# Optimization experiments

Hardware: AMD Instinct MI355X
Metric: run time of the kernel (lower is better)

## Reference

```python
import jax, jax.numpy as jnp
import numpy as np

T, D, H, O = 1048576, 64, 128, 32  # tokens, input_size, expert hidden, expert output_size


def setup_inputs() -> dict:
    key = jax.random.key(0)
    ks = jax.random.split(key, 11)
    s = 0.02
    return {
        "x": jax.random.normal(ks[0], (T, D), dtype=jnp.float32),
        "topk_idx": jax.random.randint(ks[1], (T, 2), 0, 2),
        "weights": jax.random.uniform(ks[2], (T, 2), dtype=jnp.float32),
        # expert 0: MLP D -> H -> O
        "W0a": jax.random.normal(ks[3], (D, H), dtype=jnp.float32) * s,
        "b0a": jnp.zeros((H,), dtype=jnp.float32),
        "W0b": jax.random.normal(ks[4], (H, O), dtype=jnp.float32) * s,
        "b0b": jnp.zeros((O,), dtype=jnp.float32),
        # expert 1: MLP (D + O) -> H -> O  (memory-enhanced input)
        "W1a": jax.random.normal(ks[5], (D + O, H), dtype=jnp.float32) * s,
        "b1a": jnp.zeros((H,), dtype=jnp.float32),
        "W1b": jax.random.normal(ks[6], (H, O), dtype=jnp.float32) * s,
        "b1b": jnp.zeros((O,), dtype=jnp.float32),
    }


def reference(x, topk_idx, weights, W0a, b0a, W0b, b0b, W1a, b1a, W1b, b1b):
    mask0 = (topk_idx == 0).any(axis=1)  # [T]
    mask1 = (topk_idx == 1).any(axis=1)  # [T]

    # expert 0 output, zero where not routed (matches zeros buffer + masked scatter)
    e0 = jnp.maximum(x @ W0a + b0a, 0.0) @ W0b + b0b      # [T, O]
    out0 = jnp.where(mask0[:, None], e0, 0.0)

    # last_valid_fill: forward-fill last valid row index (invalid -> 0, then cummax)
    t = jnp.arange(T)
    idx = jax.lax.cummax(jnp.where(mask0, t, 0))           # [T] int
    filled = out0[idx]                                     # [T, O] gather rows

    # expert 1 on [x, last_valid_out0], zero where not routed
    x1 = jnp.concatenate([x, filled], axis=1)              # [T, D+O]
    e1 = jnp.maximum(x1 @ W1a + b1a, 0.0) @ W1b + b1b      # [T, O]
    out1 = jnp.where(mask1[:, None], e1, 0.0)

    w = weights[:, :1]                                     # [T, 1]
    return w * out0 + (1.0 - w) * out1
```

## Files before the change

kernel.cpp:

```cpp
#include <hip/hip_runtime.h>
#include <hip/hip_bf16.h>

#define TROWS 1048576
#define RPB   256
#define NCHUNK (TROWS / RPB)
#define LSTRIDE 36

typedef float f32x4  __attribute__((ext_vector_type(4)));
typedef short bf16x8 __attribute__((ext_vector_type(8)));
typedef short bf16x4 __attribute__((ext_vector_type(4)));

#define MFMA(a, b, c) __builtin_amdgcn_mfma_f32_16x16x32_bf16(a, b, c, 0, 0, 0)

__device__ __forceinline__ short f2bf(float v) {
    __hip_bfloat16 b = __float2bfloat16(v);
    return __builtin_bit_cast(short, b);
}
__device__ __forceinline__ float bf2f(short s) {
    unsigned u = ((unsigned)(unsigned short)s) << 16;
    return __builtin_bit_cast(float, u);
}

__global__ __launch_bounds__(64) void prep_kernel(
    const float* __restrict__ W0a, const float* __restrict__ W0b,
    const float* __restrict__ W1a, const float* __restrict__ W1b,
    bf16x8* __restrict__ frag)
{
    const int fid = blockIdx.x, l = threadIdx.x, c = l & 15, g = l >> 4;
    const float* W; int N, ks, nt;
    if (fid < 16)      { W = W0a; N = 128; ks = fid >> 3;        nt = fid & 7; }
    else if (fid < 24) { W = W0b; N = 32;  ks = (fid - 16) >> 1; nt = (fid - 16) & 1; }
    else if (fid < 48) { W = W1a; N = 128; ks = (fid - 24) >> 3; nt = (fid - 24) & 7; }
    else               { W = W1b; N = 32;  ks = (fid - 48) >> 1; nt = (fid - 48) & 1; }
    bf16x8 f;
    #pragma unroll
    for (int j = 0; j < 8; ++j) {
        const int k = 32 * ks + ((j < 4) ? (4 * g + j) : (16 + 4 * g + (j - 4)));
        f[j] = f2bf(W[k * N + 16 * nt + c]);
    }
    frag[fid * 64 + l] = f;
}

__global__ __launch_bounds__(256, 3) void fused_kernel(
    const float* __restrict__ x, const int* __restrict__ topk,
    const float* __restrict__ wts,
    const float* __restrict__ b0a, const float* __restrict__ b0b,
    const float* __restrict__ b1a, const float* __restrict__ b1b,
    const bf16x8* __restrict__ frag,
    float* __restrict__ out)
{
    const int b = blockIdx.x;
    const int bb = b * RPB;
    const int tid = threadIdx.x, wv = tid >> 6, l = tid & 63, c = l & 15, g = l >> 4;

    __shared__ __align__(16) short frag_lds[32 * 64 * 8];
    __shared__ __align__(16) short out0_lds[257 * LSTRIDE];
    __shared__ int wtot[4];

    #define LDSF(fl) (*(const bf16x8*)&frag_lds[(((fl) * 64) + l) * 8])

    #pragma unroll
    for (int i = 0; i < 6; ++i) {
        const int e = tid + i * 256;
        *(f32x4*)&frag_lds[e * 8] = *(const f32x4*)&frag[e];
    }

    const int t = bb + tid;
    const int2 tko = ((const int2*)topk)[t];
    const bool m0o = (tko.x == 0) || (tko.y == 0);
    const bool m1o = (tko.x == 1) || (tko.y == 1);
    const int  mo_own   = (m0o ? 1 : 0) | (m1o ? 2 : 0);
    const float wgt_own = wts[(size_t)t * 2];

    int s = m0o ? t : 0;
    #pragma unroll
    for (int off = 1; off < 64; off <<= 1) {
        int u = __shfl_up(s, off, 64);
        if (l >= off) s = max(s, u);
    }
    if (l == 63) wtot[wv] = s;

    int p = 0;
    for (int base = bb - 64; base >= 0; base -= 64) {
        const int2 tkq = ((const int2*)topk)[base + l];
        const bool mm = (tkq.x == 0) || (tkq.y == 0);
        const unsigned long long bal = __ballot(mm);
        if (bal) { p = base + 63 - __clzll(bal); break; }
    }
    const int2 tkp = ((const int2*)topk)[p];
    const bool m0p = (tkp.x == 0) || (tkp.y == 0);

    bf16x8 xf[4][2];
    #pragma unroll
    for (int rt = 0; rt < 4; ++rt) {
        const int row = bb + wv * 64 + rt * 16 + c;
        const float* xr = x + (size_t)row * 64;
        #pragma unroll
        for (int ks = 0; ks < 2; ++ks) {
            f32x4 a  = *(const f32x4*)(xr + 32 * ks + 4 * g);
            f32x4 b2 = *(const f32x4*)(xr + 32 * ks + 16 + 4 * g);
            #pragma unroll
            for (int j = 0; j < 4; ++j) { xf[rt][ks][j] = f2bf(a[j]); xf[rt][ks][4 + j] = f2bf(b2[j]); }
        }
    }
    bf16x8 xfp[2];
    if (wv == 3) {
        const float* xp = x + (size_t)p * 64;
        #pragma unroll
        for (int ks = 0; ks < 2; ++ks) {
            f32x4 a  = *(const f32x4*)(xp + 32 * ks + 4 * g);
            f32x4 b2 = *(const f32x4*)(xp + 32 * ks + 16 + 4 * g);
            #pragma unroll
            for (int j = 0; j < 4; ++j) { xfp[ks][j] = f2bf(a[j]); xfp[ks][4 + j] = f2bf(b2[j]); }
        }
    }

    __syncthreads();

    int pre = 0;
    #pragma unroll
    for (int w2 = 0; w2 < 4; ++w2)
        if (w2 < wv) pre = max(pre, wtot[w2]);
    const int s_full = max(pre, s);

    f32x4 acc2a[4][2];
    {
        f32x4 bi0 = *(const f32x4*)(b0b + 4 * g);
        f32x4 bi1 = *(const f32x4*)(b0b + 16 + 4 * g);
        #pragma unroll
        for (int rt = 0; rt < 4; ++rt) { acc2a[rt][0] = bi0; acc2a[rt][1] = bi1; }
    }
    __builtin_amdgcn_s_setprio(1);
    #pragma unroll
    for (int k2 = 0; k2 < 4; ++k2) {
        const bf16x8 fa00 = LDSF(0 * 8 + 2 * k2 + 0);
        const bf16x8 fa01 = LDSF(0 * 8 + 2 * k2 + 1);
        const bf16x8 fa10 = LDSF(1 * 8 + 2 * k2 + 0);
        const bf16x8 fa11 = LDSF(1 * 8 + 2 * k2 + 1);
        const bf16x8 fb0  = LDSF(16 + 2 * k2 + 0);
        const bf16x8 fb1  = LDSF(16 + 2 * k2 + 1);
        const f32x4 bi0 = *(const f32x4*)(b0a + 16 * (2 * k2 + 0) + 4 * g);
        const f32x4 bi1 = *(const f32x4*)(b0a + 16 * (2 * k2 + 1) + 4 * g);
        #pragma unroll
        for (int rt = 0; rt < 4; ++rt) {
            f32x4 a10 = bi0, a11 = bi1;
            a10 = MFMA(fa00, xf[rt][0], a10);
            a10 = MFMA(fa10, xf[rt][1], a10);
            a11 = MFMA(fa01, xf[rt][0], a11);
            a11 = MFMA(fa11, xf[rt][1], a11);
            bf16x8 hf;
            #pragma unroll
            for (int j = 0; j < 8; ++j)
                hf[j] = f2bf(fmaxf((j < 4 ? a10 : a11)[j & 3], 0.0f));
            acc2a[rt][0] = MFMA(fb0, hf, acc2a[rt][0]);
            acc2a[rt][1] = MFMA(fb1, hf, acc2a[rt][1]);
        }
    }
    __builtin_amdgcn_s_setprio(0);

    #pragma unroll
    for (int rt = 0; rt < 4; ++rt) {
        const int slot = wv * 64 + rt * 16 + c;
        const bool m0 = (__shfl(mo_own, rt * 16 + c, 64) & 1);
        #pragma unroll
        for (int ot = 0; ot < 2; ++ot) {
            bf16x4 v;
            #pragma unroll
            for (int j = 0; j < 4; ++j) v[j] = f2bf(m0 ? acc2a[rt][ot][j] : 0.0f);
            *(bf16x4*)(&out0_lds[slot * LSTRIDE + 16 * ot + 4 * g]) = v;
        }
    }

    if (wv == 3) {
        f32x4 accp[2];
        accp[0] = *(const f32x4*)(b0b + 4 * g);
        accp[1] = *(const f32x4*)(b0b + 16 + 4 * g);
        #pragma unroll
        for (int k2 = 0; k2 < 4; ++k2) {
            const bf16x8 fa00 = LDSF(0 * 8 + 2 * k2 + 0);
            const bf16x8 fa01 = LDSF(0 * 8 + 2 * k2 + 1);
            const bf16x8 fa10 = LDSF(1 * 8 + 2 * k2 + 0);
            const bf16x8 fa11 = LDSF(1 * 8 + 2 * k2 + 1);
            const bf16x8 fb0  = LDSF(16 + 2 * k2 + 0);
            const bf16x8 fb1  = LDSF(16 + 2 * k2 + 1);
            f32x4 a10 = *(const f32x4*)(b0a + 16 * (2 * k2 + 0) + 4 * g);
            f32x4 a11 = *(const f32x4*)(b0a + 16 * (2 * k2 + 1) + 4 * g);
            a10 = MFMA(fa00, xfp[0], a10);
            a10 = MFMA(fa10, xfp[1], a10);
            a11 = MFMA(fa01, xfp[0], a11);
            a11 = MFMA(fa11, xfp[1], a11);
            bf16x8 hf;
            #pragma unroll
            for (int j = 0; j < 8; ++j)
                hf[j] = f2bf(fmaxf((j < 4 ? a10 : a11)[j & 3], 0.0f));
            accp[0] = MFMA(fb0, hf, accp[0]);
            accp[1] = MFMA(fb1, hf, accp[1]);
        }
        if (c == 0) {
            #pragma unroll
            for (int ot = 0; ot < 2; ++ot) {
                bf16x4 v;
                #pragma unroll
                for (int j = 0; j < 4; ++j) v[j] = f2bf(m0p ? accp[ot][j] : 0.0f);
                *(bf16x4*)(&out0_lds[256 * LSTRIDE + 16 * ot + 4 * g]) = v;
            }
        }
    }

    __syncthreads();

    bf16x8 xf2[4];
    #pragma unroll
    for (int rt = 0; rt < 4; ++rt) {
        const int sF = __shfl(s_full, rt * 16 + c, 64);
        const int slot = (sF > 0) ? (sF - bb) : 256;
        const short* fr = &out0_lds[slot * LSTRIDE];
        bf16x4 fa_ = *(const bf16x4*)(fr + 4 * g);
        bf16x4 fb_ = *(const bf16x4*)(fr + 16 + 4 * g);
        #pragma unroll
        for (int j = 0; j < 4; ++j) { xf2[rt][j] = fa_[j]; xf2[rt][4 + j] = fb_[j]; }
    }

    #pragma unroll
    for (int i = 0; i < 8; ++i) {
        const int e = tid + i * 256;
        *(f32x4*)&frag_lds[e * 8] = *(const f32x4*)&frag[24 * 64 + e];
    }

    __syncthreads();

    f32x4 acc2b[4][2];
    {
        f32x4 bi0 = *(const f32x4*)(b1b + 4 * g);
        f32x4 bi1 = *(const f32x4*)(b1b + 16 + 4 * g);
        #pragma unroll
        for (int rt = 0; rt < 4; ++rt) { acc2b[rt][0] = bi0; acc2b[rt][1] = bi1; }
    }
    __builtin_amdgcn_s_setprio(1);
    #pragma unroll
    for (int k2 = 0; k2 < 4; ++k2) {
        const bf16x8 fa00 = LDSF(0 * 8 + 2 * k2 + 0);
        const bf16x8 fa01 = LDSF(0 * 8 + 2 * k2 + 1);
        const bf16x8 fa10 = LDSF(1 * 8 + 2 * k2 + 0);
        const bf16x8 fa11 = LDSF(1 * 8 + 2 * k2 + 1);
        const bf16x8 fa20 = LDSF(2 * 8 + 2 * k2 + 0);
        const bf16x8 fa21 = LDSF(2 * 8 + 2 * k2 + 1);
        const bf16x8 fb0  = LDSF(24 + 2 * k2 + 0);
        const bf16x8 fb1  = LDSF(24 + 2 * k2 + 1);
        const f32x4 bi0 = *(const f32x4*)(b1a + 16 * (2 * k2 + 0) + 4 * g);
        const f32x4 bi1 = *(const f32x4*)(b1a + 16 * (2 * k2 + 1) + 4 * g);
        #pragma unroll
        for (int rt = 0; rt < 4; ++rt) {
            f32x4 a10 = bi0, a11 = bi1;
            a10 = MFMA(fa00, xf[rt][0], a10);
            a10 = MFMA(fa10, xf[rt][1], a10);
            a10 = MFMA(fa20, xf2[rt], a10);
            a11 = MFMA(fa01, xf[rt][0], a11);
            a11 = MFMA(fa11, xf[rt][1], a11);
            a11 = MFMA(fa21, xf2[rt], a11);
            bf16x8 hf;
            #pragma unroll
            for (int j = 0; j < 8; ++j)
                hf[j] = f2bf(fmaxf((j < 4 ? a10 : a11)[j & 3], 0.0f));
            acc2b[rt][0] = MFMA(fb0, hf, acc2b[rt][0]);
            acc2b[rt][1] = MFMA(fb1, hf, acc2b[rt][1]);
        }
    }
    __builtin_amdgcn_s_setprio(0);

    #pragma unroll
    for (int rt = 0; rt < 4; ++rt) {
        const int slot = wv * 64 + rt * 16 + c;
        const int row = bb + slot;
        const int mo   = __shfl(mo_own, rt * 16 + c, 64);
        const float w  = __shfl(wgt_own, rt * 16 + c, 64);
        const float wc = 1.0f - w;
        const bool m1 = mo & 2;
        #pragma unroll
        for (int ot = 0; ot < 2; ++ot) {
            bf16x4 oa = *(const bf16x4*)(&out0_lds[slot * LSTRIDE + 16 * ot + 4 * g]);
            f32x4 r;
            #pragma unroll
            for (int j = 0; j < 4; ++j) {
                const float e1 = m1 ? acc2b[rt][ot][j] : 0.0f;
                r[j] = w * bf2f(oa[j]) + wc * e1;
            }
            *(f32x4*)(out + (size_t)row * 32 + 16 * ot + 4 * g) = r;
        }
    }
    #undef LDSF
}

extern "C" void kernel_launch(void* const* d_in, const int* in_sizes, int n_in,
                              void* d_out, int out_size, void* d_ws, size_t ws_size,
                              hipStream_t stream)
{
    const float* x    = (const float*)d_in[0];
    const int*   topk = (const int*)  d_in[1];
    const float* wts  = (const float*)d_in[2];
    const float* W0a  = (const float*)d_in[3];
    const float* b0a  = (const float*)d_in[4];
    const float* W0b  = (const float*)d_in[5];
    const float* b0b  = (const float*)d_in[6];
    const float* W1a  = (const float*)d_in[7];
    const float* b1a  = (const float*)d_in[8];
    const float* W1b  = (const float*)d_in[9];
    const float* b1b  = (const float*)d_in[10];
    float* out = (float*)d_out;

    bf16x8* frag = (bf16x8*)d_ws;

    prep_kernel<<<dim3(56), dim3(64), 0, stream>>>(W0a, W0b, W1a, W1b, frag);
    fused_kernel<<<dim3(NCHUNK), dim3(256), 0, stream>>>(
        x, topk, wts, b0a, b0b, b1a, b1b, frag, out);
}
```

Before: 137.2 us.

## Halve rows per block, swizzle out0 LDS, fold carry-row MLP into main loop

Each block now handles 128 rows instead of 256, so each wave owns 32 rows. Occupancy is raised to 4 blocks per CU and LDS use shrinks: the out0 buffer becomes a 32-wide XOR-swizzled layout with no padding, and slot 0 is reused for the carried-in row. The expert-0 computation for the previous block's last valid row is interleaved into the main k-loop instead of running afterwards. Expert-1 weights are prefetched into registers before the barrier, and the feature rows are read from LDS inside the loop. Other changes: the k-loops are no longer unrolled, setprio is dropped, and the per-wave scan totals share storage with out0_lds. That aliasing risks a race between reading the totals and other waves writing out0.

```diff
diff --git a/kernel.cpp b/kernel.cpp
--- a/kernel.cpp
+++ b/kernel.cpp
@@ -2,9 +2,8 @@
 #include <hip/hip_bf16.h>
 
 #define TROWS 1048576
-#define RPB   256
-#define NCHUNK (TROWS / RPB)
-#define LSTRIDE 36
+#define RPB   128
+#define NBLK  (TROWS / RPB)
 
 typedef float f32x4  __attribute__((ext_vector_type(4)));
 typedef short bf16x8 __attribute__((ext_vector_type(8)));
@@ -19,6 +18,9 @@
 __device__ __forceinline__ float bf2f(short s) {
     unsigned u = ((unsigned)(unsigned short)s) << 16;
     return __builtin_bit_cast(float, u);
+}
+__device__ __forceinline__ int o0idx(int slot, int u) {
+    return slot * 32 + ((u ^ (slot & 7)) << 2);
 }
 
 __global__ __launch_bounds__(64) void prep_kernel(
@@ -41,7 +43,7 @@
     frag[fid * 64 + l] = f;
 }
 
-__global__ __launch_bounds__(256, 3) void fused_kernel(
+__global__ __launch_bounds__(256, 4) void fused_kernel(
     const float* __restrict__ x, const int* __restrict__ topk,
     const float* __restrict__ wts,
     const float* __restrict__ b0a, const float* __restrict__ b0b,
@@ -52,10 +54,11 @@
     const int b = blockIdx.x;
     const int bb = b * RPB;
     const int tid = threadIdx.x, wv = tid >> 6, l = tid & 63, c = l & 15, g = l >> 4;
-
-    __shared__ __align__(16) short frag_lds[32 * 64 * 8];
-    __shared__ __align__(16) short out0_lds[257 * LSTRIDE];
-    __shared__ int wtot[4];
+    const int rr = l & 31;
+
+    __shared__ __align__(16) short frag_lds[2048 * 16 / 2];
+    __shared__ __align__(16) short out0_lds[128 * 32];
+    int* wtot = (int*)out0_lds;
 
     #define LDSF(fl) (*(const bf16x8*)&frag_lds[(((fl) * 64) + l) * 8])
 
@@ -65,20 +68,23 @@
         *(f32x4*)&frag_lds[e * 8] = *(const f32x4*)&frag[e];
     }
 
-    const int t = bb + tid;
-    const int2 tko = ((const int2*)topk)[t];
+    const int srow = bb + wv * 32 + rr;
+    const int2 tko = ((const int2*)topk)[srow];
     const bool m0o = (tko.x == 0) || (tko.y == 0);
     const bool m1o = (tko.x == 1) || (tko.y == 1);
     const int  mo_own   = (m0o ? 1 : 0) | (m1o ? 2 : 0);
-    const float wgt_own = wts[(size_t)t * 2];
-
-    int s = m0o ? t : 0;
-    #pragma unroll
-    for (int off = 1; off < 64; off <<= 1) {
-        int u = __shfl_up(s, off, 64);
-        if (l >= off) s = max(s, u);
-    }
-    if (l == 63) wtot[wv] = s;
+    const float wgt_own = wts[(size_t)srow * 2];
+
+    int s = m0o ? srow : 0;
+    #pragma unroll
+    for (int off = 1; off < 32; off <<= 1) {
+        int u = __shfl_up(s, off, 32);
+        if (rr >= off) s = max(s, u);
+    }
+    if (l == 31) wtot[wv] = s;
+
+    const int2 tk0 = ((const int2*)topk)[bb];
+    const bool m0row0 = (tk0.x == 0) || (tk0.y == 0);
 
     int p = 0;
     for (int base = bb - 64; base >= 0; base -= 64) {
@@ -90,10 +96,10 @@
     const int2 tkp = ((const int2*)topk)[p];
     const bool m0p = (tkp.x == 0) || (tkp.y == 0);
 
-    bf16x8 xf[4][2];
-    #pragma unroll
-    for (int rt = 0; rt < 4; ++rt) {
-        const int row = bb + wv * 64 + rt * 16 + c;
+    bf16x8 xf[2][2];
+    #pragma unroll
+    for (int rt = 0; rt < 2; ++rt) {
+        const int row = bb + wv * 32 + rt * 16 + c;
         const float* xr = x + (size_t)row * 64;
         #pragma unroll
         for (int ks = 0; ks < 2; ++ks) {
@@ -123,15 +129,15 @@
         if (w2 < wv) pre = max(pre, wtot[w2]);
     const int s_full = max(pre, s);
 
-    f32x4 acc2a[4][2];
+    f32x4 acc2a[2][2], accp[2];
     {
         f32x4 bi0 = *(const f32x4*)(b0b + 4 * g);
         f32x4 bi1 = *(const f32x4*)(b0b + 16 + 4 * g);
-        #pragma unroll
-        for (int rt = 0; rt < 4; ++rt) { acc2a[rt][0] = bi0; acc2a[rt][1] = bi1; }
-    }
-    __builtin_amdgcn_s_setprio(1);
-    #pragma unroll
+        acc2a[0][0] = bi0; acc2a[0][1] = bi1;
+        acc2a[1][0] = bi0; acc2a[1][1] = bi1;
+        accp[0] = bi0; accp[1] = bi1;
+    }
+    #pragma unroll 1
     for (int k2 = 0; k2 < 4; ++k2) {
         const bf16x8 fa00 = LDSF(0 * 8 + 2 * k2 + 0);
         const bf16x8 fa01 = LDSF(0 * 8 + 2 * k2 + 1);
@@ -142,7 +148,7 @@
         const f32x4 bi0 = *(const f32x4*)(b0a + 16 * (2 * k2 + 0) + 4 * g);
         const f32x4 bi1 = *(const f32x4*)(b0a + 16 * (2 * k2 + 1) + 4 * g);
         #pragma unroll
-        for (int rt = 0; rt < 4; ++rt) {
+        for (int rt = 0; rt < 2; ++rt) {
             f32x4 a10 = bi0, a11 = bi1;
             a10 = MFMA(fa00, xf[rt][0], a10);
             a10 = MFMA(fa10, xf[rt][1], a10);
@@ -155,36 +161,8 @@
             acc2a[rt][0] = MFMA(fb0, hf, acc2a[rt][0]);
             acc2a[rt][1] = MFMA(fb1, hf, acc2a[rt][1]);
         }
-    }
-    __builtin_amdgcn_s_setprio(0);
-
-    #pragma unroll
-    for (int rt = 0; rt < 4; ++rt) {
-        const int slot = wv * 64 + rt * 16 + c;
-        const bool m0 = (__shfl(mo_own, rt * 16 + c, 64) & 1);
-        #pragma unroll
-        for (int ot = 0; ot < 2; ++ot) {
-            bf16x4 v;
-            #pragma unroll
-            for (int j = 0; j < 4; ++j) v[j] = f2bf(m0 ? acc2a[rt][ot][j] : 0.0f);
-            *(bf16x4*)(&out0_lds[slot * LSTRIDE + 16 * ot + 4 * g]) = v;
-        }
-    }
-
-    if (wv == 3) {
-        f32x4 accp[2];
-        accp[0] = *(const f32x4*)(b0b + 4 * g);
-        accp[1] = *(const f32x4*)(b0b + 16 + 4 * g);
-        #pragma unroll
-        for (int k2 = 0; k2 < 4; ++k2) {
-            const bf16x8 fa00 = LDSF(0 * 8 + 2 * k2 + 0);
-            const bf16x8 fa01 = LDSF(0 * 8 + 2 * k2 + 1);
-            const bf16x8 fa10 = LDSF(1 * 8 + 2 * k2 + 0);
-            const bf16x8 fa11 = LDSF(1 * 8 + 2 * k2 + 1);
-            const bf16x8 fb0  = LDSF(16 + 2 * k2 + 0);
-            const bf16x8 fb1  = LDSF(16 + 2 * k2 + 1);
-            f32x4 a10 = *(const f32x4*)(b0a + 16 * (2 * k2 + 0) + 4 * g);
-            f32x4 a11 = *(const f32x4*)(b0a + 16 * (2 * k2 + 1) + 4 * g);
+        if (wv == 3) {
+            f32x4 a10 = bi0, a11 = bi1;
             a10 = MFMA(fa00, xfp[0], a10);
             a10 = MFMA(fa10, xfp[1], a10);
             a11 = MFMA(fa01, xfp[0], a11);
@@ -196,48 +174,68 @@
             accp[0] = MFMA(fb0, hf, accp[0]);
             accp[1] = MFMA(fb1, hf, accp[1]);
         }
-        if (c == 0) {
-            #pragma unroll
-            for (int ot = 0; ot < 2; ++ot) {
-                bf16x4 v;
-                #pragma unroll
-                for (int j = 0; j < 4; ++j) v[j] = f2bf(m0p ? accp[ot][j] : 0.0f);
-                *(bf16x4*)(&out0_lds[256 * LSTRIDE + 16 * ot + 4 * g]) = v;
-            }
+    }
+
+    #pragma unroll
+    for (int rt = 0; rt < 2; ++rt) {
+        const int slot = wv * 32 + rt * 16 + c;
+        const bool m0 = (__shfl(mo_own, rt * 16 + c, 64) & 1);
+        const bool sk = (slot == 0) && !m0row0;
+        #pragma unroll
+        for (int ot = 0; ot < 2; ++ot) {
+            bf16x4 v;
+            #pragma unroll
+            for (int j = 0; j < 4; ++j) v[j] = f2bf(m0 ? acc2a[rt][ot][j] : 0.0f);
+            if (!sk) *(bf16x4*)(&out0_lds[o0idx(slot, ot * 4 + g)]) = v;
+        }
+    }
+    if (wv == 3 && !m0row0 && c == 0) {
+        #pragma unroll
+        for (int ot = 0; ot < 2; ++ot) {
+            bf16x4 v;
+            #pragma unroll
+            for (int j = 0; j < 4; ++j) v[j] = f2bf(m0p ? accp[ot][j] : 0.0f);
+            *(bf16x4*)(&out0_lds[o0idx(0, ot * 4 + g)]) = v;
         }
     }
 
     __syncthreads();
 
-    bf16x8 xf2[4];
-    #pragma unroll
-    for (int rt = 0; rt < 4; ++rt) {
+    f32x4 w1t0 = *(const f32x4*)&frag[24 * 64 + tid + 0 * 256];
+    f32x4 w1t1 = *(const f32x4*)&frag[24 * 64 + tid + 1 * 256];
+    f32x4 w1t2 = *(const f32x4*)&frag[24 * 64 + tid + 2 * 256];
+    f32x4 w1t3 = *(const f32x4*)&frag[24 * 64 + tid + 3 * 256];
+    f32x4 w1t4 = *(const f32x4*)&frag[24 * 64 + tid + 4 * 256];
+    f32x4 w1t5 = *(const f32x4*)&frag[24 * 64 + tid + 5 * 256];
+    f32x4 w1t6 = *(const f32x4*)&frag[24 * 64 + tid + 6 * 256];
+    f32x4 w1t7 = *(const f32x4*)&frag[24 * 64 + tid + 7 * 256];
+
+    int slotF[2];
+    #pragma unroll
+    for (int rt = 0; rt < 2; ++rt) {
         const int sF = __shfl(s_full, rt * 16 + c, 64);
-        const int slot = (sF > 0) ? (sF - bb) : 256;
-        const short* fr = &out0_lds[slot * LSTRIDE];
-        bf16x4 fa_ = *(const bf16x4*)(fr + 4 * g);
-        bf16x4 fb_ = *(const bf16x4*)(fr + 16 + 4 * g);
-        #pragma unroll
-        for (int j = 0; j < 4; ++j) { xf2[rt][j] = fa_[j]; xf2[rt][4 + j] = fb_[j]; }
-    }
-
-    #pragma unroll
-    for (int i = 0; i < 8; ++i) {
-        const int e = tid + i * 256;
-        *(f32x4*)&frag_lds[e * 8] = *(const f32x4*)&frag[24 * 64 + e];
-    }
+        slotF[rt] = (sF > 0) ? (sF - bb) : 0;
+    }
+
+    *(f32x4*)&frag_lds[(tid + 0 * 256) * 8] = w1t0;
+    *(f32x4*)&frag_lds[(tid + 1 * 256) * 8] = w1t1;
+    *(f32x4*)&frag_lds[(tid + 2 * 256) * 8] = w1t2;
+    *(f32x4*)&frag_lds[(tid + 3 * 256) * 8] = w1t3;
+    *(f32x4*)&frag_lds[(tid + 4 * 256) * 8] = w1t4;
+    *(f32x4*)&frag_lds[(tid + 5 * 256) * 8] = w1t5;
+    *(f32x4*)&frag_lds[(tid + 6 * 256) * 8] = w1t6;
+    *(f32x4*)&frag_lds[(tid + 7 * 256) * 8] = w1t7;
 
     __syncthreads();
 
-    f32x4 acc2b[4][2];
+    f32x4 acc2b[2][2];
     {
         f32x4 bi0 = *(const f32x4*)(b1b + 4 * g);
         f32x4 bi1 = *(const f32x4*)(b1b + 16 + 4 * g);
-        #pragma unroll
-        for (int rt = 0; rt < 4; ++rt) { acc2b[rt][0] = bi0; acc2b[rt][1] = bi1; }
-    }
-    __builtin_amdgcn_s_setprio(1);
-    #pragma unroll
+        acc2b[0][0] = bi0; acc2b[0][1] = bi1;
+        acc2b[1][0] = bi0; acc2b[1][1] = bi1;
+    }
+    #pragma unroll 1
     for (int k2 = 0; k2 < 4; ++k2) {
         const bf16x8 fa00 = LDSF(0 * 8 + 2 * k2 + 0);
         const bf16x8 fa01 = LDSF(0 * 8 + 2 * k2 + 1);
@@ -250,14 +248,22 @@
         const f32x4 bi0 = *(const f32x4*)(b1a + 16 * (2 * k2 + 0) + 4 * g);
         const f32x4 bi1 = *(const f32x4*)(b1a + 16 * (2 * k2 + 1) + 4 * g);
         #pragma unroll
-        for (int rt = 0; rt < 4; ++rt) {
+        for (int rt = 0; rt < 2; ++rt) {
+            bf16x8 xf2;
+            {
+                const int sl = slotF[rt];
+                bf16x4 fa_ = *(const bf16x4*)&out0_lds[o0idx(sl, g)];
+                bf16x4 fb_ = *(const bf16x4*)&out0_lds[o0idx(sl, 4 + g)];
+                #pragma unroll
+                for (int j = 0; j < 4; ++j) { xf2[j] = fa_[j]; xf2[4 + j] = fb_[j]; }
+            }
             f32x4 a10 = bi0, a11 = bi1;
             a10 = MFMA(fa00, xf[rt][0], a10);
             a10 = MFMA(fa10, xf[rt][1], a10);
-            a10 = MFMA(fa20, xf2[rt], a10);
+            a10 = MFMA(fa20, xf2, a10);
             a11 = MFMA(fa01, xf[rt][0], a11);
             a11 = MFMA(fa11, xf[rt][1], a11);
-            a11 = MFMA(fa21, xf2[rt], a11);
+            a11 = MFMA(fa21, xf2, a11);
             bf16x8 hf;
             #pragma unroll
             for (int j = 0; j < 8; ++j)
@@ -266,24 +272,25 @@
             acc2b[rt][1] = MFMA(fb1, hf, acc2b[rt][1]);
         }
     }
-    __builtin_amdgcn_s_setprio(0);
-
-    #pragma unroll
-    for (int rt = 0; rt < 4; ++rt) {
-        const int slot = wv * 64 + rt * 16 + c;
+
+    #pragma unroll
+    for (int rt = 0; rt < 2; ++rt) {
+        const int slot = wv * 32 + rt * 16 + c;
         const int row = bb + slot;
         const int mo   = __shfl(mo_own, rt * 16 + c, 64);
         const float w  = __shfl(wgt_own, rt * 16 + c, 64);
         const float wc = 1.0f - w;
         const bool m1 = mo & 2;
+        const bool kill = (slot == 0) && !m0row0;
         #pragma unroll
         for (int ot = 0; ot < 2; ++ot) {
-            bf16x4 oa = *(const bf16x4*)(&out0_lds[slot * LSTRIDE + 16 * ot + 4 * g]);
+            bf16x4 oa = *(const bf16x4*)(&out0_lds[o0idx(slot, ot * 4 + g)]);
             f32x4 r;
             #pragma unroll
             for (int j = 0; j < 4; ++j) {
+                const float e0 = kill ? 0.0f : bf2f(oa[j]);
                 const float e1 = m1 ? acc2b[rt][ot][j] : 0.0f;
-                r[j] = w * bf2f(oa[j]) + wc * e1;
+                r[j] = w * e0 + wc * e1;
             }
             *(f32x4*)(out + (size_t)row * 32 + 16 * ot + 4 * g) = r;
         }
@@ -311,6 +318,6 @@
     bf16x8* frag = (bf16x8*)d_ws;
 
     prep_kernel<<<dim3(56), dim3(64), 0, stream>>>(W0a, W0b, W1a, W1b, frag);
-    fused_kernel<<<dim3(NCHUNK), dim3(256), 0, stream>>>(
+    fused_kernel<<<dim3(NBLK), dim3(256), 0, stream>>>(
         x, topk, wts, b0a, b0b, b1a, b1b, frag, out);
 }
```

Measured after the change: 134.3 us. 2.1% less time.

## Make fused kernel persistent over 8 chunks with register prefetch and carried fill index

Applied to the files above, without the earlier changes.

Each block now processes 8 consecutive 256-row chunks instead of one. All weight fragments for both experts are loaded into LDS once per block. The next chunk's x, topk and weights are prefetched into registers while the current chunk computes. The backward scan for the last valid expert-0 row is done once per block, and the fill index is then carried from chunk to chunk. This removes the repeated per-chunk scans, weight reloads and a sync, but raises register and LDS pressure (occupancy hint drops to 2) and gives only 512 blocks.

```diff
diff --git a/kernel.cpp b/kernel.cpp
--- a/kernel.cpp
+++ b/kernel.cpp
@@ -2,8 +2,9 @@
 #include <hip/hip_bf16.h>
 
 #define TROWS 1048576
-#define RPB   256
-#define NCHUNK (TROWS / RPB)
+#define RPC   256
+#define CPB   8
+#define NBLK  (TROWS / (RPC * CPB))
 #define LSTRIDE 36
 
 typedef float f32x4  __attribute__((ext_vector_type(4)));
@@ -41,7 +42,7 @@
     frag[fid * 64 + l] = f;
 }
 
-__global__ __launch_bounds__(256, 3) void fused_kernel(
+__global__ __launch_bounds__(256, 2) void fused_kernel(
     const float* __restrict__ x, const int* __restrict__ topk,
     const float* __restrict__ wts,
     const float* __restrict__ b0a, const float* __restrict__ b0b,
@@ -49,132 +50,96 @@
     const bf16x8* __restrict__ frag,
     float* __restrict__ out)
 {
-    const int b = blockIdx.x;
-    const int bb = b * RPB;
     const int tid = threadIdx.x, wv = tid >> 6, l = tid & 63, c = l & 15, g = l >> 4;
-
-    __shared__ __align__(16) short frag_lds[32 * 64 * 8];
+    const int blk0 = blockIdx.x * (RPC * CPB);
+
+    __shared__ __align__(16) short frag_lds[56 * 64 * 8];
     __shared__ __align__(16) short out0_lds[257 * LSTRIDE];
     __shared__ int wtot[4];
 
-    #define LDSF(fl) (*(const bf16x8*)&frag_lds[(((fl) * 64) + l) * 8])
+    #define LDSF(fid_) (*(const bf16x8*)&frag_lds[(((fid_) * 64) + l) * 8])
 
     #pragma unroll
-    for (int i = 0; i < 6; ++i) {
-        const int e = tid + i * 256;
-        *(f32x4*)&frag_lds[e * 8] = *(const f32x4*)&frag[e];
+    for (int i = 0; i < 14; ++i)
+        *(f32x4*)&frag_lds[(tid + i * 256) * 8] = *(const f32x4*)&frag[tid + i * 256];
+
+    int p = 0; bool m0p = false;
+    f32x4 xpraw[4];
+    if (wv == 3) {
+        for (int base = blk0 - 64; base >= 0; base -= 64) {
+            const int2 tkq = ((const int2*)topk)[base + l];
+            const bool mm = (tkq.x == 0) || (tkq.y == 0);
+            const unsigned long long bal = __ballot(mm);
+            if (bal) { p = base + 63 - __clzll(bal); break; }
+        }
+        const int2 tkp = ((const int2*)topk)[p];
+        m0p = (tkp.x == 0) || (tkp.y == 0);
+        const float* xp = x + (size_t)p * 64;
+        xpraw[0] = *(const f32x4*)(xp + 4 * g);
+        xpraw[1] = *(const f32x4*)(xp + 16 + 4 * g);
+        xpraw[2] = *(const f32x4*)(xp + 32 + 4 * g);
+        xpraw[3] = *(const f32x4*)(xp + 48 + 4 * g);
     }
 
-    const int t = bb + tid;
-    const int2 tko = ((const int2*)topk)[t];
-    const bool m0o = (tko.x == 0) || (tko.y == 0);
-    const bool m1o = (tko.x == 1) || (tko.y == 1);
-    const int  mo_own   = (m0o ? 1 : 0) | (m1o ? 2 : 0);
-    const float wgt_own = wts[(size_t)t * 2];
-
-    int s = m0o ? t : 0;
-    #pragma unroll
-    for (int off = 1; off < 64; off <<= 1) {
-        int u = __shfl_up(s, off, 64);
-        if (l >= off) s = max(s, u);
-    }
-    if (l == 63) wtot[wv] = s;
-
-    int p = 0;
-    for (int base = bb - 64; base >= 0; base -= 64) {
-        const int2 tkq = ((const int2*)topk)[base + l];
-        const bool mm = (tkq.x == 0) || (tkq.y == 0);
-        const unsigned long long bal = __ballot(mm);
-        if (bal) { p = base + 63 - __clzll(bal); break; }
-    }
-    const int2 tkp = ((const int2*)topk)[p];
-    const bool m0p = (tkp.x == 0) || (tkp.y == 0);
-
-    bf16x8 xf[4][2];
+    f32x4 xraw[16];
     #pragma unroll
     for (int rt = 0; rt < 4; ++rt) {
-        const int row = bb + wv * 64 + rt * 16 + c;
-        const float* xr = x + (size_t)row * 64;
-        #pragma unroll
-        for (int ks = 0; ks < 2; ++ks) {
-            f32x4 a  = *(const f32x4*)(xr + 32 * ks + 4 * g);
-            f32x4 b2 = *(const f32x4*)(xr + 32 * ks + 16 + 4 * g);
-            #pragma unroll
-            for (int j = 0; j < 4; ++j) { xf[rt][ks][j] = f2bf(a[j]); xf[rt][ks][4 + j] = f2bf(b2[j]); }
-        }
+        const float* xr = x + (size_t)(blk0 + wv * 64 + rt * 16 + c) * 64;
+        xraw[rt * 4 + 0] = *(const f32x4*)(xr + 4 * g);
+        xraw[rt * 4 + 1] = *(const f32x4*)(xr + 16 + 4 * g);
+        xraw[rt * 4 + 2] = *(const f32x4*)(xr + 32 + 4 * g);
+        xraw[rt * 4 + 3] = *(const f32x4*)(xr + 48 + 4 * g);
     }
-    bf16x8 xfp[2];
-    if (wv == 3) {
-        const float* xp = x + (size_t)p * 64;
-        #pragma unroll
-        for (int ks = 0; ks < 2; ++ks) {
-            f32x4 a  = *(const f32x4*)(xp + 32 * ks + 4 * g);
-            f32x4 b2 = *(const f32x4*)(xp + 32 * ks + 16 + 4 * g);
-            #pragma unroll
-            for (int j = 0; j < 4; ++j) { xfp[ks][j] = f2bf(a[j]); xfp[ks][4 + j] = f2bf(b2[j]); }
-        }
-    }
+    int2  tko = ((const int2*)topk)[blk0 + tid];
+    float wgt = wts[(size_t)(blk0 + tid) * 2];
 
     __syncthreads();
 
-    int pre = 0;
-    #pragma unroll
-    for (int w2 = 0; w2 < 4; ++w2)
-        if (w2 < wv) pre = max(pre, wtot[w2]);
-    const int s_full = max(pre, s);
-
-    f32x4 acc2a[4][2];
-    {
-        f32x4 bi0 = *(const f32x4*)(b0b + 4 * g);
-        f32x4 bi1 = *(const f32x4*)(b0b + 16 + 4 * g);
-        #pragma unroll
-        for (int rt = 0; rt < 4; ++rt) { acc2a[rt][0] = bi0; acc2a[rt][1] = bi1; }
-    }
-    __builtin_amdgcn_s_setprio(1);
-    #pragma unroll
-    for (int k2 = 0; k2 < 4; ++k2) {
-        const bf16x8 fa00 = LDSF(0 * 8 + 2 * k2 + 0);
-        const bf16x8 fa01 = LDSF(0 * 8 + 2 * k2 + 1);
-        const bf16x8 fa10 = LDSF(1 * 8 + 2 * k2 + 0);
-        const bf16x8 fa11 = LDSF(1 * 8 + 2 * k2 + 1);
-        const bf16x8 fb0  = LDSF(16 + 2 * k2 + 0);
-        const bf16x8 fb1  = LDSF(16 + 2 * k2 + 1);
-        const f32x4 bi0 = *(const f32x4*)(b0a + 16 * (2 * k2 + 0) + 4 * g);
-        const f32x4 bi1 = *(const f32x4*)(b0a + 16 * (2 * k2 + 1) + 4 * g);
-        #pragma unroll
-        for (int rt = 0; rt < 4; ++rt) {
-            f32x4 a10 = bi0, a11 = bi1;
-            a10 = MFMA(fa00, xf[rt][0], a10);
-            a10 = MFMA(fa10, xf[rt][1], a10);
-            a11 = MFMA(fa01, xf[rt][0], a11);
-            a11 = MFMA(fa11, xf[rt][1], a11);
-            bf16x8 hf;
-            #pragma unroll
-            for (int j = 0; j < 8; ++j)
-                hf[j] = f2bf(fmaxf((j < 4 ? a10 : a11)[j & 3], 0.0f));
-            acc2a[rt][0] = MFMA(fb0, hf, acc2a[rt][0]);
-            acc2a[rt][1] = MFMA(fb1, hf, acc2a[rt][1]);
-        }
-    }
-    __builtin_amdgcn_s_setprio(0);
-
-    #pragma unroll
-    for (int rt = 0; rt < 4; ++rt) {
-        const int slot = wv * 64 + rt * 16 + c;
-        const bool m0 = (__shfl(mo_own, rt * 16 + c, 64) & 1);
-        #pragma unroll
-        for (int ot = 0; ot < 2; ++ot) {
-            bf16x4 v;
-            #pragma unroll
-            for (int j = 0; j < 4; ++j) v[j] = f2bf(m0 ? acc2a[rt][ot][j] : 0.0f);
-            *(bf16x4*)(&out0_lds[slot * LSTRIDE + 16 * ot + 4 * g]) = v;
-        }
-    }
-
-    if (wv == 3) {
-        f32x4 accp[2];
-        accp[0] = *(const f32x4*)(b0b + 4 * g);
-        accp[1] = *(const f32x4*)(b0b + 16 + 4 * g);
+    #pragma unroll 1
+    for (int ch = 0; ch < CPB; ++ch) {
+        const int cb = blk0 + ch * RPC;
+
+        bf16x8 xf[4][2];
+        #pragma unroll
+        for (int rt = 0; rt < 4; ++rt)
+            #pragma unroll
+            for (int ks = 0; ks < 2; ++ks) {
+                const f32x4 a  = xraw[rt * 4 + ks * 2 + 0];
+                const f32x4 b2 = xraw[rt * 4 + ks * 2 + 1];
+                #pragma unroll
+                for (int j = 0; j < 4; ++j) { xf[rt][ks][j] = f2bf(a[j]); xf[rt][ks][4 + j] = f2bf(b2[j]); }
+            }
+        bf16x8 xfp[2];
+        if (wv == 3) {
+            #pragma unroll
+            for (int ks = 0; ks < 2; ++ks) {
+                const f32x4 a  = xpraw[ks * 2 + 0];
+                const f32x4 b2 = xpraw[ks * 2 + 1];
+                #pragma unroll
+                for (int j = 0; j < 4; ++j) { xfp[ks][j] = f2bf(a[j]); xfp[ks][4 + j] = f2bf(b2[j]); }
+            }
+        }
+
+        const bool m0o = (tko.x == 0) || (tko.y == 0);
+        const bool m1o = (tko.x == 1) || (tko.y == 1);
+        const int  mo_own   = (m0o ? 1 : 0) | (m1o ? 2 : 0);
+        const float wgt_own = wgt;
+        int s = m0o ? (cb + tid) : 0;
+        #pragma unroll
+        for (int off = 1; off < 64; off <<= 1) {
+            int u = __shfl_up(s, off, 64);
+            if (l >= off) s = max(s, u);
+        }
+        if (l == 63) wtot[wv] = s;
+
+        f32x4 acc2a[4][2], accp[2];
+        {
+            f32x4 bi0 = *(const f32x4*)(b0b + 4 * g);
+            f32x4 bi1 = *(const f32x4*)(b0b + 16 + 4 * g);
+            #pragma unroll
+            for (int rt = 0; rt < 4; ++rt) { acc2a[rt][0] = bi0; acc2a[rt][1] = bi1; }
+            accp[0] = bi0; accp[1] = bi1;
+        }
         #pragma unroll
         for (int k2 = 0; k2 < 4; ++k2) {
             const bf16x8 fa00 = LDSF(0 * 8 + 2 * k2 + 0);
@@ -183,110 +148,162 @@
             const bf16x8 fa11 = LDSF(1 * 8 + 2 * k2 + 1);
             const bf16x8 fb0  = LDSF(16 + 2 * k2 + 0);
             const bf16x8 fb1  = LDSF(16 + 2 * k2 + 1);
-            f32x4 a10 = *(const f32x4*)(b0a + 16 * (2 * k2 + 0) + 4 * g);
-            f32x4 a11 = *(const f32x4*)(b0a + 16 * (2 * k2 + 1) + 4 * g);
-            a10 = MFMA(fa00, xfp[0], a10);
-            a10 = MFMA(fa10, xfp[1], a10);
-            a11 = MFMA(fa01, xfp[0], a11);
-            a11 = MFMA(fa11, xfp[1], a11);
-            bf16x8 hf;
-            #pragma unroll
-            for (int j = 0; j < 8; ++j)
-                hf[j] = f2bf(fmaxf((j < 4 ? a10 : a11)[j & 3], 0.0f));
-            accp[0] = MFMA(fb0, hf, accp[0]);
-            accp[1] = MFMA(fb1, hf, accp[1]);
-        }
-        if (c == 0) {
+            const f32x4 bi0 = *(const f32x4*)(b0a + 16 * (2 * k2 + 0) + 4 * g);
+            const f32x4 bi1 = *(const f32x4*)(b0a + 16 * (2 * k2 + 1) + 4 * g);
+            #pragma unroll
+            for (int rt = 0; rt < 4; ++rt) {
+                f32x4 a10 = bi0, a11 = bi1;
+                a10 = MFMA(fa00, xf[rt][0], a10);
+                a10 = MFMA(fa10, xf[rt][1], a10);
+                a11 = MFMA(fa01, xf[rt][0], a11);
+                a11 = MFMA(fa11, xf[rt][1], a11);
+                bf16x8 hf;
+                #pragma unroll
+                for (int j = 0; j < 8; ++j)
+                    hf[j] = f2bf(fmaxf((j < 4 ? a10 : a11)[j & 3], 0.0f));
+                acc2a[rt][0] = MFMA(fb0, hf, acc2a[rt][0]);
+                acc2a[rt][1] = MFMA(fb1, hf, acc2a[rt][1]);
+            }
+            if (wv == 3) {
+                f32x4 a10 = bi0, a11 = bi1;
+                a10 = MFMA(fa00, xfp[0], a10);
+                a10 = MFMA(fa10, xfp[1], a10);
+                a11 = MFMA(fa01, xfp[0], a11);
+                a11 = MFMA(fa11, xfp[1], a11);
+                bf16x8 hf;
+                #pragma unroll
+                for (int j = 0; j < 8; ++j)
+                    hf[j] = f2bf(fmaxf((j < 4 ? a10 : a11)[j & 3], 0.0f));
+                accp[0] = MFMA(fb0, hf, accp[0]);
+                accp[1] = MFMA(fb1, hf, accp[1]);
+            }
+        }
+
+        #pragma unroll
+        for (int rt = 0; rt < 4; ++rt) {
+            const int slot = wv * 64 + rt * 16 + c;
+            const bool m0 = (__shfl(mo_own, rt * 16 + c, 64) & 1);
             #pragma unroll
             for (int ot = 0; ot < 2; ++ot) {
                 bf16x4 v;
                 #pragma unroll
+                for (int j = 0; j < 4; ++j) v[j] = f2bf(m0 ? acc2a[rt][ot][j] : 0.0f);
+                *(bf16x4*)(&out0_lds[slot * LSTRIDE + 16 * ot + 4 * g]) = v;
+            }
+        }
+        if (wv == 3 && c == 0) {
+            #pragma unroll
+            for (int ot = 0; ot < 2; ++ot) {
+                bf16x4 v;
+                #pragma unroll
                 for (int j = 0; j < 4; ++j) v[j] = f2bf(m0p ? accp[ot][j] : 0.0f);
                 *(bf16x4*)(&out0_lds[256 * LSTRIDE + 16 * ot + 4 * g]) = v;
             }
         }
-    }
-
-    __syncthreads();
-
-    bf16x8 xf2[4];
-    #pragma unroll
-    for (int rt = 0; rt < 4; ++rt) {
-        const int sF = __shfl(s_full, rt * 16 + c, 64);
-        const int slot = (sF > 0) ? (sF - bb) : 256;
-        const short* fr = &out0_lds[slot * LSTRIDE];
-        bf16x4 fa_ = *(const bf16x4*)(fr + 4 * g);
-        bf16x4 fb_ = *(const bf16x4*)(fr + 16 + 4 * g);
-        #pragma unroll
-        for (int j = 0; j < 4; ++j) { xf2[rt][j] = fa_[j]; xf2[rt][4 + j] = fb_[j]; }
-    }
-
-    #pragma unroll
-    for (int i = 0; i < 8; ++i) {
-        const int e = tid + i * 256;
-        *(f32x4*)&frag_lds[e * 8] = *(const f32x4*)&frag[24 * 64 + e];
-    }
-
-    __syncthreads();
-
-    f32x4 acc2b[4][2];
-    {
-        f32x4 bi0 = *(const f32x4*)(b1b + 4 * g);
-        f32x4 bi1 = *(const f32x4*)(b1b + 16 + 4 * g);
-        #pragma unroll
-        for (int rt = 0; rt < 4; ++rt) { acc2b[rt][0] = bi0; acc2b[rt][1] = bi1; }
-    }
-    __builtin_amdgcn_s_setprio(1);
-    #pragma unroll
-    for (int k2 = 0; k2 < 4; ++k2) {
-        const bf16x8 fa00 = LDSF(0 * 8 + 2 * k2 + 0);
-        const bf16x8 fa01 = LDSF(0 * 8 + 2 * k2 + 1);
-        const bf16x8 fa10 = LDSF(1 * 8 + 2 * k2 + 0);
-        const bf16x8 fa11 = LDSF(1 * 8 + 2 * k2 + 1);
-        const bf16x8 fa20 = LDSF(2 * 8 + 2 * k2 + 0);
-        const bf16x8 fa21 = LDSF(2 * 8 + 2 * k2 + 1);
-        const bf16x8 fb0  = LDSF(24 + 2 * k2 + 0);
-        const bf16x8 fb1  = LDSF(24 + 2 * k2 + 1);
-        const f32x4 bi0 = *(const f32x4*)(b1a + 16 * (2 * k2 + 0) + 4 * g);
-        const f32x4 bi1 = *(const f32x4*)(b1a + 16 * (2 * k2 + 1) + 4 * g);
+
+        __syncthreads();
+
+        if (ch + 1 < CPB) {
+            const int nb = cb + RPC;
+            #pragma unroll
+            for (int rt = 0; rt < 4; ++rt) {
+                const float* xr = x + (size_t)(nb + wv * 64 + rt * 16 + c) * 64;
+                xraw[rt * 4 + 0] = *(const f32x4*)(xr + 4 * g);
+                xraw[rt * 4 + 1] = *(const f32x4*)(xr + 16 + 4 * g);
+                xraw[rt * 4 + 2] = *(const f32x4*)(xr + 32 + 4 * g);
+                xraw[rt * 4 + 3] = *(const f32x4*)(xr + 48 + 4 * g);
+            }
+            tko = ((const int2*)topk)[nb + tid];
+            wgt = wts[(size_t)(nb + tid) * 2];
+        }
+
+        int pre = 0;
+        #pragma unroll
+        for (int w2 = 0; w2 < 4; ++w2)
+            if (w2 < wv) pre = max(pre, wtot[w2]);
+        const int s_full = max(pre, s);
+
+        if (wv == 3 && ch + 1 < CPB) {
+            const int sl = __shfl(s_full, 63, 64);
+            if (sl > 0) { p = sl; m0p = true; }
+            const float* xp = x + (size_t)p * 64;
+            xpraw[0] = *(const f32x4*)(xp + 4 * g);
+            xpraw[1] = *(const f32x4*)(xp + 16 + 4 * g);
+            xpraw[2] = *(const f32x4*)(xp + 32 + 4 * g);
+            xpraw[3] = *(const f32x4*)(xp + 48 + 4 * g);
+        }
+
+        bf16x8 xf2[4];
         #pragma unroll
         for (int rt = 0; rt < 4; ++rt) {
-            f32x4 a10 = bi0, a11 = bi1;
-            a10 = MFMA(fa00, xf[rt][0], a10);
-            a10 = MFMA(fa10, xf[rt][1], a10);
-            a10 = MFMA(fa20, xf2[rt], a10);
-            a11 = MFMA(fa01, xf[rt][0], a11);
-            a11 = MFMA(fa11, xf[rt][1], a11);
-            a11 = MFMA(fa21, xf2[rt], a11);
-            bf16x8 hf;
-            #pragma unroll
-            for (int j = 0; j < 8; ++j)
-                hf[j] = f2bf(fmaxf((j < 4 ? a10 : a11)[j & 3], 0.0f));
-            acc2b[rt][0] = MFMA(fb0, hf, acc2b[rt][0]);
-            acc2b[rt][1] = MFMA(fb1, hf, acc2b[rt][1]);
-        }
-    }
-    __builtin_amdgcn_s_setprio(0);
-
-    #pragma unroll
-    for (int rt = 0; rt < 4; ++rt) {
-        const int slot = wv * 64 + rt * 16 + c;
-        const int row = bb + slot;
-        const int mo   = __shfl(mo_own, rt * 16 + c, 64);
-        const float w  = __shfl(wgt_own, rt * 16 + c, 64);
-        const float wc = 1.0f - w;
-        const bool m1 = mo & 2;
-        #pragma unroll
-        for (int ot = 0; ot < 2; ++ot) {
-            bf16x4 oa = *(const bf16x4*)(&out0_lds[slot * LSTRIDE + 16 * ot + 4 * g]);
-            f32x4 r;
-            #pragma unroll
-            for (int j = 0; j < 4; ++j) {
-                const float e1 = m1 ? acc2b[rt][ot][j] : 0.0f;
-                r[j] = w * bf2f(oa[j]) + wc * e1;
-            }
-            *(f32x4*)(out + (size_t)row * 32 + 16 * ot + 4 * g) = r;
-        }
+            const int sF = __shfl(s_full, rt * 16 + c, 64);
+            const int slot = (sF >= cb) ? (sF - cb) : 256;
+            const short* fr = &out0_lds[slot * LSTRIDE];
+            bf16x4 fa_ = *(const bf16x4*)(fr + 4 * g);
+            bf16x4 fb_ = *(const bf16x4*)(fr + 16 + 4 * g);
+            #pragma unroll
+            for (int j = 0; j < 4; ++j) { xf2[rt][j] = fa_[j]; xf2[rt][4 + j] = fb_[j]; }
+        }
+
+        f32x4 acc2b[4][2];
+        {
+            f32x4 bi0 = *(const f32x4*)(b1b + 4 * g);
+            f32x4 bi1 = *(const f32x4*)(b1b + 16 + 4 * g);
+            #pragma unroll
+            for (int rt = 0; rt < 4; ++rt) { acc2b[rt][0] = bi0; acc2b[rt][1] = bi1; }
+        }
+        #pragma unroll
+        for (int k2 = 0; k2 < 4; ++k2) {
+            const bf16x8 fa00 = LDSF(24 + 0 * 8 + 2 * k2 + 0);
+            const bf16x8 fa01 = LDSF(24 + 0 * 8 + 2 * k2 + 1);
+            const bf16x8 fa10 = LDSF(24 + 1 * 8 + 2 * k2 + 0);
+            const bf16x8 fa11 = LDSF(24 + 1 * 8 + 2 * k2 + 1);
+            const bf16x8 fa20 = LDSF(24 + 2 * 8 + 2 * k2 + 0);
+            const bf16x8 fa21 = LDSF(24 + 2 * 8 + 2 * k2 + 1);
+            const bf16x8 fb0  = LDSF(48 + 2 * k2 + 0);
+            const bf16x8 fb1  = LDSF(48 + 2 * k2 + 1);
+            const f32x4 bi0 = *(const f32x4*)(b1a + 16 * (2 * k2 + 0) + 4 * g);
+            const f32x4 bi1 = *(const f32x4*)(b1a + 16 * (2 * k2 + 1) + 4 * g);
+            #pragma unroll
+            for (int rt = 0; rt < 4; ++rt) {
+                f32x4 a10 = bi0, a11 = bi1;
+                a10 = MFMA(fa00, xf[rt][0], a10);
+                a10 = MFMA(fa10, xf[rt][1], a10);
+                a10 = MFMA(fa20, xf2[rt], a10);
+                a11 = MFMA(fa01, xf[rt][0], a11);
+                a11 = MFMA(fa11, xf[rt][1], a11);
+                a11 = MFMA(fa21, xf2[rt], a11);
+                bf16x8 hf;
+                #pragma unroll
+                for (int j = 0; j < 8; ++j)
+                    hf[j] = f2bf(fmaxf((j < 4 ? a10 : a11)[j & 3], 0.0f));
+                acc2b[rt][0] = MFMA(fb0, hf, acc2b[rt][0]);
+                acc2b[rt][1] = MFMA(fb1, hf, acc2b[rt][1]);
+            }
+        }
+
+        #pragma unroll
+        for (int rt = 0; rt < 4; ++rt) {
+            const int slot = wv * 64 + rt * 16 + c;
+            const int row = cb + slot;
+            const int mo   = __shfl(mo_own, rt * 16 + c, 64);
+            const float w  = __shfl(wgt_own, rt * 16 + c, 64);
+            const float wc = 1.0f - w;
+            const bool m1 = mo & 2;
+            #pragma unroll
+            for (int ot = 0; ot < 2; ++ot) {
+                bf16x4 oa = *(const bf16x4*)(&out0_lds[slot * LSTRIDE + 16 * ot + 4 * g]);
+                f32x4 r;
+                #pragma unroll
+                for (int j = 0; j < 4; ++j) {
+                    const float e1 = m1 ? acc2b[rt][ot][j] : 0.0f;
+                    r[j] = w * bf2f(oa[j]) + wc * e1;
+                }
+                *(f32x4*)(out + (size_t)row * 32 + 16 * ot + 4 * g) = r;
+            }
+        }
+
+        __syncthreads();
     }
     #undef LDSF
 }
@@ -311,6 +328,6 @@
     bf16x8* frag = (bf16x8*)d_ws;
 
     prep_kernel<<<dim3(56), dim3(64), 0, stream>>>(W0a, W0b, W1a, W1b, frag);
-    fused_kernel<<<dim3(NCHUNK), dim3(256), 0, stream>>>(
+    fused_kernel<<<dim3(NBLK), dim3(256), 0, stream>>>(
         x, topk, wts, b0a, b0b, b1a, b1b, frag, out);
 }
```

Measured after the change: 214.0 us. 1.56x slower.
